# Kernel tuning notes

Hardware: AMD Instinct MI355X
Metric: run time of the kernel (lower is better)

The kernel has to match this reference:

```python
import jax, jax.numpy as jnp
import numpy as np

H = 1024   # hidden_size
B = 4096   # batch
C = 2      # num_classes

def setup_inputs() -> dict:
    key = jax.random.key(0)
    ks = jax.random.split(key, 12)
    s = 0.02
    return {
        "h": jax.random.normal(ks[0], (2, B, H), jnp.float32),
        "c": jax.random.normal(ks[1], (2, B, H), jnp.float32),
        # torch nn.LSTM params: W_ih_l0 (4H, C), W_hh_l0 (4H, H), biases (4H,)
        "W_ih0": jax.random.normal(ks[2], (4 * H, C), jnp.float32) * s,
        "W_hh0": jax.random.normal(ks[3], (4 * H, H), jnp.float32) * s,
        "b_ih0": jax.random.normal(ks[4], (4 * H,), jnp.float32) * s,
        "b_hh0": jax.random.normal(ks[5], (4 * H,), jnp.float32) * s,
        "W_ih1": jax.random.normal(ks[6], (4 * H, H), jnp.float32) * s,
        "W_hh1": jax.random.normal(ks[7], (4 * H, H), jnp.float32) * s,
        "b_ih1": jax.random.normal(ks[8], (4 * H,), jnp.float32) * s,
        "b_hh1": jax.random.normal(ks[9], (4 * H,), jnp.float32) * s,
        "fc_W": jax.random.normal(ks[10], (C, H), jnp.float32) * s,
        "fc_b": jax.random.normal(ks[11], (C,), jnp.float32) * s,
        "pred_len": 64,
    }

def _lstm_cell(gates, c_prev):
    # torch gate order: input, forget, cell(g), output
    i, f, g, o = jnp.split(gates, 4, axis=1)
    c_new = jax.nn.sigmoid(f) * c_prev + jax.nn.sigmoid(i) * jnp.tanh(g)
    h_new = jax.nn.sigmoid(o) * jnp.tanh(c_new)
    return h_new, c_new

def reference(h, c, W_ih0, W_hh0, b_ih0, b_hh0, W_ih1, W_hh1, b_ih1, b_hh1, fc_W, fc_b, pred_len):
    h0, h1 = h[0], h[1]
    c0, c1 = c[0], c[1]
    x0 = jnp.zeros((h0.shape[0], fc_W.shape[0]), h.dtype)  # (B, C)

    def step(carry, _):
        h0, c0, h1, c1, x = carry
        g0 = x @ W_ih0.T + b_ih0 + h0 @ W_hh0.T + b_hh0
        h0n, c0n = _lstm_cell(g0, c0)
        g1 = h0n @ W_ih1.T + b_ih1 + h1 @ W_hh1.T + b_hh1
        h1n, c1n = _lstm_cell(g1, c1)
        logit = h1n @ fc_W.T + fc_b                       # (B, C)
        # greedy argmax feedback (targets=None branch)
        x_next = jax.nn.one_hot(jnp.argmax(logit, axis=1), logit.shape[1], dtype=logit.dtype)
        return (h0n, c0n, h1n, c1n, x_next), logit

    _, logits = jax.lax.scan(step, (h0, c0, h1, c1, x0), None, length=pred_len)
    return jnp.transpose(logits, (1, 0, 2))  # (B, pred_len, C)
```

## Files before the change

### kernel.cpp

```cpp
#include <hip/hip_runtime.h>
#include <stdint.h>

#define H_ 1024
#define NG_ 4096

typedef float f32x4 __attribute__((ext_vector_type(4)));
typedef __bf16 bf16x8 __attribute__((ext_vector_type(8)));

__device__ __forceinline__ unsigned short f2bf(float f) {
  union { float f; uint32_t u; } v; v.f = f;
  uint32_t r = v.u + 0x7FFFu + ((v.u >> 16) & 1u);
  return (unsigned short)(r >> 16);
}
__device__ __forceinline__ float bf2f(unsigned short b) {
  union { uint32_t u; float f; } v; v.u = ((uint32_t)b) << 16; return v.f;
}

__device__ __forceinline__ void gload_lds16(const void* g, void* l) {
  __builtin_amdgcn_global_load_lds(
      (const __attribute__((address_space(1))) void*)g,
      (__attribute__((address_space(3))) void*)l, 16, 0, 0);
}

__device__ __forceinline__ float sigm(float x) { return 1.f / (1.f + __expf(-x)); }
__device__ __forceinline__ float tanh_(float x) { return 1.f - 2.f / (__expf(2.f * x) + 1.f); }

__global__ void prep_w0(const float* __restrict__ Whh0, unsigned short* __restrict__ Wr) {
  int i = (blockIdx.x * 256 + threadIdx.x) * 4;
  int r = i >> 10, k = i & 1023;
  int gate = (r >> 4) & 3;
  int j = ((r >> 6) << 4) + (r & 15);
  const float4 v = *(const float4*)(Whh0 + (size_t)(gate * H_ + j) * H_ + k);
  ushort4 o; o.x = f2bf(v.x); o.y = f2bf(v.y); o.z = f2bf(v.z); o.w = f2bf(v.w);
  *(ushort4*)(Wr + i) = o;
}

__global__ void prep_wcat(const float* __restrict__ Wih1, const float* __restrict__ Whh1,
                          unsigned short* __restrict__ Wr) {
  int i = (blockIdx.x * 256 + threadIdx.x) * 4;
  int r = i >> 11, k = i & 2047;
  int gate = (r >> 4) & 3;
  int j = ((r >> 6) << 4) + (r & 15);
  const float* src = (k < 1024) ? (Wih1 + (size_t)(gate * H_ + j) * H_ + k)
                                : (Whh1 + (size_t)(gate * H_ + j) * H_ + (k - 1024));
  const float4 v = *(const float4*)src;
  ushort4 o; o.x = f2bf(v.x); o.y = f2bf(v.y); o.z = f2bf(v.z); o.w = f2bf(v.w);
  *(ushort4*)(Wr + (size_t)r * 2048 + k) = o;
}

__global__ void prep_small(const float* __restrict__ Wih0,
                           const float* __restrict__ bih0, const float* __restrict__ bhh0,
                           const float* __restrict__ bih1, const float* __restrict__ bhh1,
                           float* __restrict__ bias0r, float* __restrict__ bias1r,
                           float* __restrict__ wi0r) {
  int r = blockIdx.x * 256 + threadIdx.x;
  int gate = (r >> 4) & 3;
  int j = ((r >> 6) << 4) + (r & 15);
  int old = gate * H_ + j;
  bias0r[r] = bih0[old] + bhh0[old];
  bias1r[r] = bih1[old] + bhh1[old];
  wi0r[r * 2 + 0] = Wih0[old * 2 + 0];
  wi0r[r * 2 + 1] = Wih0[old * 2 + 1];
}

__global__ void prep_state(const float* __restrict__ h, const float* __restrict__ c,
                           unsigned short* __restrict__ h0b, unsigned short* __restrict__ h1b,
                           float* __restrict__ c0, float* __restrict__ c1, int bh) {
  int i = (blockIdx.x * 256 + threadIdx.x) * 4;
  float4 a = *(const float4*)(h + i);
  float4 b = *(const float4*)(h + (size_t)bh + i);
  ushort4 oa; oa.x = f2bf(a.x); oa.y = f2bf(a.y); oa.z = f2bf(a.z); oa.w = f2bf(a.w);
  ushort4 ob; ob.x = f2bf(b.x); ob.y = f2bf(b.y); ob.z = f2bf(b.z); ob.w = f2bf(b.w);
  *(ushort4*)(h0b + i) = oa;
  *(ushort4*)(h1b + i) = ob;
  *(float4*)(c0 + i) = *(const float4*)(c + i);
  *(float4*)(c1 + i) = *(const float4*)(c + (size_t)bh + i);
}

__global__ void __launch_bounds__(512, 2)
lstm_gemm_cell(const unsigned short* __restrict__ A0,
               const unsigned short* __restrict__ A1,
               int Ktot,
               const unsigned short* __restrict__ Bw,
               const float* __restrict__ biasr,
               const float* __restrict__ wi0r,
               const int* __restrict__ xidx,
               int have_x,
               float* __restrict__ Cst,
               unsigned short* __restrict__ Hout) {
  __shared__ unsigned short As[2][256 * 64];
  __shared__ unsigned short Bs[2][256 * 64];

  const int tid  = threadIdx.x;
  const int lane = tid & 63;
  const int wv   = tid >> 6;
  const int wm   = wv >> 2;
  const int wn   = wv & 3;
  const int tile_m = blockIdx.y * 256;
  const int tile_n = blockIdx.x * 256;

  const int rowt = tid >> 3;
  const int cb8  = (tid & 7) * 8;
  const int ce   = (((tid & 7) ^ (rowt & 7)) * 8);

  const int NK = Ktot >> 6;

  auto stage = [&](int d, int kt) {
    const int kb = kt << 6;
    const unsigned short* Ap = A0; int kl = kb;
    if (kb >= 1024) { Ap = A1; kl = kb - 1024; }
#pragma unroll
    for (int i = 0; i < 4; ++i) {
      const int row = i * 64 + rowt;
      gload_lds16(Ap + (size_t)(tile_m + row) * H_ + kl + ce, (void*)&As[d][row * 64 + cb8]);
    }
#pragma unroll
    for (int i = 0; i < 4; ++i) {
      const int row = i * 64 + rowt;
      gload_lds16(Bw + (size_t)(tile_n + row) * (size_t)Ktot + kb + ce, (void*)&Bs[d][row * 64 + cb8]);
    }
  };

  f32x4 acc[8][4];
#pragma unroll
  for (int m = 0; m < 8; ++m)
#pragma unroll
    for (int n = 0; n < 4; ++n) acc[m][n] = (f32x4)0.f;

  const int cl  = lane & 15;
  const int khi = lane >> 4;
  const int Xn  = lane & 7;
  const int ksw0 = ((0 + khi) ^ Xn) * 16;
  const int ksw1 = ((4 + khi) ^ Xn) * 16;

  stage(0, 0);
  stage(1, 1);
  asm volatile("s_waitcnt vmcnt(8)" ::: "memory");
  __builtin_amdgcn_sched_barrier(0);
  __builtin_amdgcn_s_barrier();

  for (int kt = 0; kt < NK; ++kt) {
    const int cur = kt & 1;
    const char* Abase = (const char*)&As[cur][0] + (wm * 128 + cl) * 128;
    const char* Bbase = (const char*)&Bs[cur][0] + (wn * 64 + cl) * 128;

    bf16x8 af0[8], af1[8], bf0[4], bf1[4];
#pragma unroll
    for (int m = 0; m < 8; ++m) {
      af0[m] = *(const bf16x8*)(Abase + m * 2048 + ksw0);
      af1[m] = *(const bf16x8*)(Abase + m * 2048 + ksw1);
    }
#pragma unroll
    for (int n = 0; n < 4; ++n) {
      bf0[n] = *(const bf16x8*)(Bbase + n * 2048 + ksw0);
      bf1[n] = *(const bf16x8*)(Bbase + n * 2048 + ksw1);
    }

    asm volatile("s_waitcnt lgkmcnt(0)" ::: "memory");
    __builtin_amdgcn_sched_barrier(0);
    __builtin_amdgcn_s_barrier();

    if (kt + 2 < NK) {
      stage(cur, kt + 2);
      asm volatile("s_waitcnt vmcnt(8)" ::: "memory");
    } else {
      asm volatile("s_waitcnt vmcnt(0)" ::: "memory");
    }
    __builtin_amdgcn_sched_barrier(0);

    __builtin_amdgcn_s_setprio(1);
#pragma unroll
    for (int m = 0; m < 8; ++m)
#pragma unroll
      for (int n = 0; n < 4; ++n)
        acc[m][n] = __builtin_amdgcn_mfma_f32_16x16x32_bf16(af0[m], bf0[n], acc[m][n], 0, 0, 0);
#pragma unroll
    for (int m = 0; m < 8; ++m)
#pragma unroll
      for (int n = 0; n < 4; ++n)
        acc[m][n] = __builtin_amdgcn_mfma_f32_16x16x32_bf16(af1[m], bf1[n], acc[m][n], 0, 0, 0);
    __builtin_amdgcn_s_setprio(0);

    __builtin_amdgcn_s_barrier();
  }

  const int jgrp = (tile_n >> 6) + wn;
  const int j = jgrp * 16 + cl;
  float bias[4], w0v[4] = {0, 0, 0, 0}, w1v[4] = {0, 0, 0, 0};
#pragma unroll
  for (int n = 0; n < 4; ++n) {
    int colr = tile_n + wn * 64 + n * 16 + cl;
    bias[n] = biasr[colr];
    if (have_x) { w0v[n] = wi0r[colr * 2]; w1v[n] = wi0r[colr * 2 + 1]; }
  }
#pragma unroll
  for (int m = 0; m < 8; ++m) {
#pragma unroll
    for (int q = 0; q < 4; ++q) {
      int row = tile_m + wm * 128 + m * 16 + khi * 4 + q;
      float gi = acc[m][0][q] + bias[0];
      float gf = acc[m][1][q] + bias[1];
      float gg = acc[m][2][q] + bias[2];
      float go = acc[m][3][q] + bias[3];
      if (have_x) {
        int x = xidx[row];
        gi += x ? w1v[0] : w0v[0];
        gf += x ? w1v[1] : w0v[1];
        gg += x ? w1v[2] : w0v[2];
        go += x ? w1v[3] : w0v[3];
      }
      size_t off = (size_t)row * H_ + j;
      float cp = Cst[off];
      float cn = sigm(gf) * cp + sigm(gi) * tanh_(gg);
      float hn = sigm(go) * tanh_(cn);
      Cst[off] = cn;
      Hout[off] = f2bf(hn);
    }
  }
}

__global__ void fc_argmax(const unsigned short* __restrict__ h1,
                          const float* __restrict__ fcW, const float* __restrict__ fcb,
                          float* __restrict__ out, int* __restrict__ xidx,
                          int t, int pred_len) {
  const int lane = threadIdx.x & 63;
  const int wv = threadIdx.x >> 6;
  const int row = blockIdx.x * 4 + wv;
  const unsigned short* hp = h1 + (size_t)row * H_ + lane * 16;
  float d0 = 0.f, d1 = 0.f;
#pragma unroll
  for (int u = 0; u < 2; ++u) {
    ushort4 ha = *(const ushort4*)(hp + u * 8);
    ushort4 hb = *(const ushort4*)(hp + u * 8 + 4);
    float hv[8] = { bf2f(ha.x), bf2f(ha.y), bf2f(ha.z), bf2f(ha.w),
                    bf2f(hb.x), bf2f(hb.y), bf2f(hb.z), bf2f(hb.w) };
#pragma unroll
    for (int e = 0; e < 8; ++e) {
      int k = lane * 16 + u * 8 + e;
      d0 += hv[e] * fcW[k];
      d1 += hv[e] * fcW[H_ + k];
    }
  }
#pragma unroll
  for (int off = 32; off > 0; off >>= 1) {
    d0 += __shfl_xor(d0, off);
    d1 += __shfl_xor(d1, off);
  }
  if (lane == 0) {
    d0 += fcb[0]; d1 += fcb[1];
    size_t o = ((size_t)row * pred_len + t) * 2;
    out[o] = d0; out[o + 1] = d1;
    xidx[row] = (d1 > d0) ? 1 : 0;
  }
}

extern "C" void kernel_launch(void* const* d_in, const int* in_sizes, int n_in,
                              void* d_out, int out_size, void* d_ws, size_t ws_size,
                              hipStream_t stream) {
  const float* h     = (const float*)d_in[0];
  const float* c     = (const float*)d_in[1];
  const float* Wih0  = (const float*)d_in[2];
  const float* Whh0  = (const float*)d_in[3];
  const float* bih0  = (const float*)d_in[4];
  const float* bhh0  = (const float*)d_in[5];
  const float* Wih1  = (const float*)d_in[6];
  const float* Whh1  = (const float*)d_in[7];
  const float* bih1  = (const float*)d_in[8];
  const float* bhh1  = (const float*)d_in[9];
  const float* fcW   = (const float*)d_in[10];
  const float* fcb   = (const float*)d_in[11];

  const int B = in_sizes[0] / (2 * H_);
  const int pred_len = out_size / (B * 2);
  const int BH = B * H_;

  size_t off = 0;
  auto carve = [&](size_t bytes) -> void* {
    void* p = (char*)d_ws + off;
    off += (bytes + 255) & ~(size_t)255;
    return p;
  };
  unsigned short* Whh0r = (unsigned short*)carve((size_t)NG_ * 1024 * 2);
  unsigned short* Wcatr = (unsigned short*)carve((size_t)NG_ * 2048 * 2);
  unsigned short* h0b[2], *h1b[2];
  h0b[0] = (unsigned short*)carve((size_t)BH * 2);
  h0b[1] = (unsigned short*)carve((size_t)BH * 2);
  h1b[0] = (unsigned short*)carve((size_t)BH * 2);
  h1b[1] = (unsigned short*)carve((size_t)BH * 2);
  float* c0 = (float*)carve((size_t)BH * 4);
  float* c1 = (float*)carve((size_t)BH * 4);
  float* bias0r = (float*)carve(NG_ * 4);
  float* bias1r = (float*)carve(NG_ * 4);
  float* wi0r   = (float*)carve(NG_ * 2 * 4);
  int*   xidx   = (int*)carve(B * 4);

  hipLaunchKernelGGL(prep_w0,   dim3((NG_ * 1024 / 4) / 256), dim3(256), 0, stream, Whh0, Whh0r);
  hipLaunchKernelGGL(prep_wcat, dim3((NG_ * 2048 / 4) / 256), dim3(256), 0, stream, Wih1, Whh1, Wcatr);
  hipLaunchKernelGGL(prep_small, dim3(NG_ / 256), dim3(256), 0, stream,
                     Wih0, bih0, bhh0, bih1, bhh1, bias0r, bias1r, wi0r);
  hipLaunchKernelGGL(prep_state, dim3((BH / 4) / 256), dim3(256), 0, stream,
                     h, c, h0b[0], h1b[0], c0, c1, BH);

  dim3 ggrid(NG_ / 256, B / 256);
  dim3 gblk(512);
  float* out = (float*)d_out;

  for (int t = 0; t < pred_len; ++t) {
    const int cur = t & 1, nxt = cur ^ 1;
    hipLaunchKernelGGL(lstm_gemm_cell, ggrid, gblk, 0, stream,
                       h0b[cur], (const unsigned short*)nullptr, 1024, Whh0r,
                       bias0r, wi0r, xidx, (t > 0) ? 1 : 0, c0, h0b[nxt]);
    hipLaunchKernelGGL(lstm_gemm_cell, ggrid, gblk, 0, stream,
                       h0b[nxt], h1b[cur], 2048, Wcatr,
                       bias1r, (const float*)nullptr, (const int*)nullptr, 0, c1, h1b[nxt]);
    hipLaunchKernelGGL(fc_argmax, dim3(B / 4), dim3(256), 0, stream,
                       h1b[nxt], fcW, fcb, out, xidx, t, pred_len);
  }
}
```

Baseline: 8.121 ms.

## Restructure GEMM main loop into 8-phase interleaved load/MFMA schedule

Replaces the two-stage per-k-tile loop with an 8-phase schedule per pair of k-tiles. Each phase reads a quarter of the A fragments from LDS, issues half of one A or B global-to-LDS stage, and runs 16 MFMAs, so global loads, LDS reads and compute are interleaved more finely. This aims to hide memory latency and cut register pressure from holding all A fragments at once. In exchange it adds more barriers per k-tile and relies on tight vmcnt accounting. At the tail it re-stages an already consumed tile, which looks questionable.

```diff
diff --git a/kernel.cpp b/kernel.cpp
--- a/kernel.cpp
+++ b/kernel.cpp
@@ -105,18 +105,23 @@
 
   const int NK = Ktot >> 6;
 
-  auto stage = [&](int d, int kt) {
-    const int kb = kt << 6;
+  auto stageA = [&](int t, int half) {
+    const int d = t & 1;
+    const int kb = t << 6;
     const unsigned short* Ap = A0; int kl = kb;
     if (kb >= 1024) { Ap = A1; kl = kb - 1024; }
 #pragma unroll
-    for (int i = 0; i < 4; ++i) {
-      const int row = i * 64 + rowt;
+    for (int i = 0; i < 2; ++i) {
+      const int row = half * 128 + i * 64 + rowt;
       gload_lds16(Ap + (size_t)(tile_m + row) * H_ + kl + ce, (void*)&As[d][row * 64 + cb8]);
     }
-#pragma unroll
-    for (int i = 0; i < 4; ++i) {
-      const int row = i * 64 + rowt;
+  };
+  auto stageB = [&](int t, int half) {
+    const int d = t & 1;
+    const int kb = t << 6;
+#pragma unroll
+    for (int i = 0; i < 2; ++i) {
+      const int row = half * 128 + i * 64 + rowt;
       gload_lds16(Bw + (size_t)(tile_n + row) * (size_t)Ktot + kb + ce, (void*)&Bs[d][row * 64 + cb8]);
     }
   };
@@ -133,56 +138,67 @@
   const int ksw0 = ((0 + khi) ^ Xn) * 16;
   const int ksw1 = ((4 + khi) ^ Xn) * 16;
 
-  stage(0, 0);
-  stage(1, 1);
-  asm volatile("s_waitcnt vmcnt(8)" ::: "memory");
+  bf16x8 bfr0[4], bfr1[4];
+
+#define DO_PHASE(T_, Q_, LOADB_, STAGE_EXPR_, TAILWAIT_)                          \
+  {                                                                               \
+    const char* Ab_ = (const char*)&As[(T_) & 1][0] + (wm * 128 + cl) * 128;      \
+    bf16x8 a00_ = *(const bf16x8*)(Ab_ + (2 * (Q_) + 0) * 2048 + ksw0);           \
+    bf16x8 a01_ = *(const bf16x8*)(Ab_ + (2 * (Q_) + 0) * 2048 + ksw1);           \
+    bf16x8 a10_ = *(const bf16x8*)(Ab_ + (2 * (Q_) + 1) * 2048 + ksw0);           \
+    bf16x8 a11_ = *(const bf16x8*)(Ab_ + (2 * (Q_) + 1) * 2048 + ksw1);           \
+    if (LOADB_) {                                                                 \
+      const char* Bb_ = (const char*)&Bs[(T_) & 1][0] + (wn * 64 + cl) * 128;     \
+      _Pragma("unroll")                                                           \
+      for (int n_ = 0; n_ < 4; ++n_) {                                            \
+        bfr0[n_] = *(const bf16x8*)(Bb_ + n_ * 2048 + ksw0);                      \
+        bfr1[n_] = *(const bf16x8*)(Bb_ + n_ * 2048 + ksw1);                      \
+      }                                                                           \
+    }                                                                             \
+    STAGE_EXPR_;                                                                  \
+    __builtin_amdgcn_s_barrier();                                                 \
+    asm volatile("s_waitcnt lgkmcnt(0)" ::: "memory");                            \
+    __builtin_amdgcn_sched_barrier(0);                                            \
+    __builtin_amdgcn_s_setprio(1);                                                \
+    _Pragma("unroll")                                                             \
+    for (int n_ = 0; n_ < 4; ++n_) {                                              \
+      acc[2*(Q_)+0][n_] = __builtin_amdgcn_mfma_f32_16x16x32_bf16(a00_, bfr0[n_], acc[2*(Q_)+0][n_], 0, 0, 0); \
+      acc[2*(Q_)+0][n_] = __builtin_amdgcn_mfma_f32_16x16x32_bf16(a01_, bfr1[n_], acc[2*(Q_)+0][n_], 0, 0, 0); \
+      acc[2*(Q_)+1][n_] = __builtin_amdgcn_mfma_f32_16x16x32_bf16(a10_, bfr0[n_], acc[2*(Q_)+1][n_], 0, 0, 0); \
+      acc[2*(Q_)+1][n_] = __builtin_amdgcn_mfma_f32_16x16x32_bf16(a11_, bfr1[n_], acc[2*(Q_)+1][n_], 0, 0, 0); \
+    }                                                                             \
+    __builtin_amdgcn_s_setprio(0);                                                \
+    if (TAILWAIT_) {                                                              \
+      asm volatile("s_waitcnt vmcnt(4)" ::: "memory");                            \
+      __builtin_amdgcn_sched_barrier(0);                                          \
+    }                                                                             \
+    __builtin_amdgcn_s_barrier();                                                 \
+  }
+
+  stageA(0, 0); stageA(0, 1);
+  stageB(0, 0); stageB(0, 1);
+  stageB(1, 0); stageB(1, 1);
+  asm volatile("s_waitcnt vmcnt(4)" ::: "memory");
   __builtin_amdgcn_sched_barrier(0);
   __builtin_amdgcn_s_barrier();
 
-  for (int kt = 0; kt < NK; ++kt) {
-    const int cur = kt & 1;
-    const char* Abase = (const char*)&As[cur][0] + (wm * 128 + cl) * 128;
-    const char* Bbase = (const char*)&Bs[cur][0] + (wn * 64 + cl) * 128;
-
-    bf16x8 af0[8], af1[8], bf0[4], bf1[4];
-#pragma unroll
-    for (int m = 0; m < 8; ++m) {
-      af0[m] = *(const bf16x8*)(Abase + m * 2048 + ksw0);
-      af1[m] = *(const bf16x8*)(Abase + m * 2048 + ksw1);
-    }
-#pragma unroll
-    for (int n = 0; n < 4; ++n) {
-      bf0[n] = *(const bf16x8*)(Bbase + n * 2048 + ksw0);
-      bf1[n] = *(const bf16x8*)(Bbase + n * 2048 + ksw1);
-    }
-
-    asm volatile("s_waitcnt lgkmcnt(0)" ::: "memory");
-    __builtin_amdgcn_sched_barrier(0);
-    __builtin_amdgcn_s_barrier();
-
-    if (kt + 2 < NK) {
-      stage(cur, kt + 2);
-      asm volatile("s_waitcnt vmcnt(8)" ::: "memory");
-    } else {
-      asm volatile("s_waitcnt vmcnt(0)" ::: "memory");
-    }
-    __builtin_amdgcn_sched_barrier(0);
-
-    __builtin_amdgcn_s_setprio(1);
-#pragma unroll
-    for (int m = 0; m < 8; ++m)
-#pragma unroll
-      for (int n = 0; n < 4; ++n)
-        acc[m][n] = __builtin_amdgcn_mfma_f32_16x16x32_bf16(af0[m], bf0[n], acc[m][n], 0, 0, 0);
-#pragma unroll
-    for (int m = 0; m < 8; ++m)
-#pragma unroll
-      for (int n = 0; n < 4; ++n)
-        acc[m][n] = __builtin_amdgcn_mfma_f32_16x16x32_bf16(af1[m], bf1[n], acc[m][n], 0, 0, 0);
-    __builtin_amdgcn_s_setprio(0);
-
-    __builtin_amdgcn_s_barrier();
-  }
+  const int NIT = NK >> 1;
+  for (int j = 0; j < NIT; ++j) {
+    const int t0 = 2 * j, t1 = 2 * j + 1;
+    const int t2 = (t0 + 2 < NK) ? t0 + 2 : t0;
+    const int t3 = (t1 + 2 < NK) ? t1 + 2 : t1;
+    DO_PHASE(t0, 0, 1, stageA(t1, 0), 0);
+    DO_PHASE(t0, 1, 0, stageA(t1, 1), 0);
+    DO_PHASE(t0, 2, 0, stageB(t2, 0), 0);
+    DO_PHASE(t0, 3, 0, stageB(t2, 1), 1);
+    DO_PHASE(t1, 0, 1, stageA(t2, 0), 0);
+    DO_PHASE(t1, 1, 0, stageA(t2, 1), 0);
+    DO_PHASE(t1, 2, 0, stageB(t3, 0), 0);
+    DO_PHASE(t1, 3, 0, stageB(t3, 1), 1);
+  }
+#undef DO_PHASE
+
+  asm volatile("s_waitcnt vmcnt(0)" ::: "memory");
 
   const int jgrp = (tile_n >> 6) + wn;
   const int j = jgrp * 16 + cl;
```

Result: no change. 8.042 ms (-1.0%).

## Interleave LDS fragment loads with MFMA in a four-phase ping-pong GEMM pipeline

Applied to the files above, without the earlier changes.

Restructures the GEMM main loop into four sub-phases, each issuing half-tile A global→LDS loads or B loads and prefetching the next register fragments while MFMAs run on the current ones. Register fragment arrays are halved, with A/B ping-pong buffers across phases. The aim is to hide LDS read latency and the global load issue behind matrix-core work instead of stalling on lgkmcnt(0) before every K step. It adds more barriers and uses clamped dummy stage indices in the tail iterations, which makes the buffer hazard reasoning fragile.

```diff
diff --git a/kernel.cpp b/kernel.cpp
--- a/kernel.cpp
+++ b/kernel.cpp
@@ -105,18 +105,23 @@
 
   const int NK = Ktot >> 6;
 
-  auto stage = [&](int d, int kt) {
-    const int kb = kt << 6;
+  auto stageA = [&](int v, int half) {
+    const int d = v & 1;
+    const int kb = v << 6;
     const unsigned short* Ap = A0; int kl = kb;
     if (kb >= 1024) { Ap = A1; kl = kb - 1024; }
 #pragma unroll
-    for (int i = 0; i < 4; ++i) {
-      const int row = i * 64 + rowt;
+    for (int i = 0; i < 2; ++i) {
+      const int row = half * 128 + i * 64 + rowt;
       gload_lds16(Ap + (size_t)(tile_m + row) * H_ + kl + ce, (void*)&As[d][row * 64 + cb8]);
     }
-#pragma unroll
-    for (int i = 0; i < 4; ++i) {
-      const int row = i * 64 + rowt;
+  };
+  auto stageB = [&](int v, int half) {
+    const int d = v & 1;
+    const int kb = v << 6;
+#pragma unroll
+    for (int i = 0; i < 2; ++i) {
+      const int row = half * 128 + i * 64 + rowt;
       gload_lds16(Bw + (size_t)(tile_n + row) * (size_t)Ktot + kb + ce, (void*)&Bs[d][row * 64 + cb8]);
     }
   };
@@ -129,60 +134,86 @@
 
   const int cl  = lane & 15;
   const int khi = lane >> 4;
-  const int Xn  = lane & 7;
-  const int ksw0 = ((0 + khi) ^ Xn) * 16;
-  const int ksw1 = ((4 + khi) ^ Xn) * 16;
-
-  stage(0, 0);
-  stage(1, 1);
-  asm volatile("s_waitcnt vmcnt(8)" ::: "memory");
+  const int ksw0 = ((0 + khi) ^ (cl & 7)) * 16;
+  const int ksw1 = ((4 + khi) ^ (cl & 7)) * 16;
+
+  const char* Ab0 = (const char*)&As[0][0] + (wm * 128 + cl) * 128;
+  const char* Bb0 = (const char*)&Bs[0][0] + (wn * 64 + cl) * 128;
+
+  bf16x8 aX[4], aY[4], bX[4], bY[4];
+
+#define MFMA16(AF, BF, MOFF)                                                         \
+  _Pragma("unroll")                                                                  \
+  for (int n_ = 0; n_ < 4; ++n_)                                                     \
+  _Pragma("unroll")                                                                  \
+  for (int i_ = 0; i_ < 4; ++i_)                                                     \
+    acc[(MOFF) + i_][n_] =                                                           \
+        __builtin_amdgcn_mfma_f32_16x16x32_bf16(AF[i_], BF[n_], acc[(MOFF) + i_][n_], 0, 0, 0);
+
+  stageA(0, 0); stageA(0, 1);
+  stageB(0, 0); stageB(0, 1);
+  stageB(1, 0); stageB(1, 1);
+  asm volatile("s_waitcnt vmcnt(4)" ::: "memory");
   __builtin_amdgcn_sched_barrier(0);
   __builtin_amdgcn_s_barrier();
-
-  for (int kt = 0; kt < NK; ++kt) {
-    const int cur = kt & 1;
-    const char* Abase = (const char*)&As[cur][0] + (wm * 128 + cl) * 128;
-    const char* Bbase = (const char*)&Bs[cur][0] + (wn * 64 + cl) * 128;
-
-    bf16x8 af0[8], af1[8], bf0[4], bf1[4];
-#pragma unroll
-    for (int m = 0; m < 8; ++m) {
-      af0[m] = *(const bf16x8*)(Abase + m * 2048 + ksw0);
-      af1[m] = *(const bf16x8*)(Abase + m * 2048 + ksw1);
-    }
-#pragma unroll
-    for (int n = 0; n < 4; ++n) {
-      bf0[n] = *(const bf16x8*)(Bbase + n * 2048 + ksw0);
-      bf1[n] = *(const bf16x8*)(Bbase + n * 2048 + ksw1);
-    }
-
-    asm volatile("s_waitcnt lgkmcnt(0)" ::: "memory");
+#pragma unroll
+  for (int i = 0; i < 4; ++i) aX[i] = *(const bf16x8*)(Ab0 + i * 2048 + ksw0);
+#pragma unroll
+  for (int n = 0; n < 4; ++n) bX[n] = *(const bf16x8*)(Bb0 + n * 2048 + ksw0);
+
+  for (int u = 0; u < NK; ++u) {
+    const char* Ab = Ab0 + (u & 1) * 32768;
+    const char* Bb = Bb0 + (u & 1) * 32768;
+    const int un = (u + 1 < NK) ? u + 1 : NK - 2;
+    const int ub = (u + 2 < NK) ? u + 2 : (((u + 2) & 1) ? NK - 1 : NK - 2);
+    const int ur = (u + 1 < NK) ? u + 1 : u;
+    const char* Abn = Ab0 + (ur & 1) * 32768;
+    const char* Bbn = Bb0 + (ur & 1) * 32768;
+
+#pragma unroll
+    for (int i = 0; i < 4; ++i) aY[i] = *(const bf16x8*)(Ab + 8192 + i * 2048 + ksw0);
+    stageA(un, 0);
+    __builtin_amdgcn_s_barrier();
+    __builtin_amdgcn_s_setprio(1);
+    MFMA16(aX, bX, 0);
+    __builtin_amdgcn_s_setprio(0);
+    __builtin_amdgcn_s_barrier();
+
+#pragma unroll
+    for (int i = 0; i < 4; ++i) aX[i] = *(const bf16x8*)(Ab + i * 2048 + ksw1);
+#pragma unroll
+    for (int n = 0; n < 4; ++n) bY[n] = *(const bf16x8*)(Bb + n * 2048 + ksw1);
+    stageA(un, 1);
+    __builtin_amdgcn_s_barrier();
+    __builtin_amdgcn_s_setprio(1);
+    MFMA16(aY, bX, 4);
+    __builtin_amdgcn_s_setprio(0);
+    __builtin_amdgcn_s_barrier();
+
+#pragma unroll
+    for (int i = 0; i < 4; ++i) aY[i] = *(const bf16x8*)(Ab + 8192 + i * 2048 + ksw1);
+    __builtin_amdgcn_s_barrier();
+    __builtin_amdgcn_s_setprio(1);
+    MFMA16(aX, bY, 0);
+    __builtin_amdgcn_s_setprio(0);
+    __builtin_amdgcn_s_barrier();
+
+    stageB(ub, 0); stageB(ub, 1);
+    asm volatile("s_waitcnt vmcnt(4)" ::: "memory");
     __builtin_amdgcn_sched_barrier(0);
     __builtin_amdgcn_s_barrier();
-
-    if (kt + 2 < NK) {
-      stage(cur, kt + 2);
-      asm volatile("s_waitcnt vmcnt(8)" ::: "memory");
-    } else {
-      asm volatile("s_waitcnt vmcnt(0)" ::: "memory");
-    }
-    __builtin_amdgcn_sched_barrier(0);
-
+#pragma unroll
+    for (int i = 0; i < 4; ++i) aX[i] = *(const bf16x8*)(Abn + i * 2048 + ksw0);
+#pragma unroll
+    for (int n = 0; n < 4; ++n) bX[n] = *(const bf16x8*)(Bbn + n * 2048 + ksw0);
     __builtin_amdgcn_s_setprio(1);
-#pragma unroll
-    for (int m = 0; m < 8; ++m)
-#pragma unroll
-      for (int n = 0; n < 4; ++n)
-        acc[m][n] = __builtin_amdgcn_mfma_f32_16x16x32_bf16(af0[m], bf0[n], acc[m][n], 0, 0, 0);
-#pragma unroll
-    for (int m = 0; m < 8; ++m)
-#pragma unroll
-      for (int n = 0; n < 4; ++n)
-        acc[m][n] = __builtin_amdgcn_mfma_f32_16x16x32_bf16(af1[m], bf1[n], acc[m][n], 0, 0, 0);
+    MFMA16(aY, bY, 4);
     __builtin_amdgcn_s_setprio(0);
-
-    __builtin_amdgcn_s_barrier();
-  }
+    __builtin_amdgcn_s_barrier();
+  }
+#undef MFMA16
+
+  asm volatile("s_waitcnt vmcnt(0) lgkmcnt(0)" ::: "memory");
 
   const int jgrp = (tile_n >> 6) + wn;
   const int j = jgrp * 16 + cl;
```

Result: slower. 9.221 ms (+13.5%).

## Load weight fragments directly from global memory and halve the N tile

Applied to the files above, without the earlier changes.

The GEMM-cell kernel no longer stages weight tiles in LDS. Each wave reads its bf16 weight fragments straight from global memory, while only the activation tile goes through double-buffered LDS. The N tile shrinks from 256 to 128, giving twice as many blocks, and launch bounds are raised to allow 4 blocks per CU with a smaller accumulator set. Nontemporal stores are used for the bf16 weights, state and h outputs. The trade-off is fewer LDS bytes and more occupancy against uncoalesced 16-byte global reads of weights and less reuse per block.

```diff
diff --git a/kernel.cpp b/kernel.cpp
--- a/kernel.cpp
+++ b/kernel.cpp
@@ -6,6 +6,7 @@
 
 typedef float f32x4 __attribute__((ext_vector_type(4)));
 typedef __bf16 bf16x8 __attribute__((ext_vector_type(8)));
+typedef unsigned short us4 __attribute__((ext_vector_type(4)));
 
 __device__ __forceinline__ unsigned short f2bf(float f) {
   union { float f; uint32_t u; } v; v.f = f;
@@ -31,8 +32,8 @@
   int gate = (r >> 4) & 3;
   int j = ((r >> 6) << 4) + (r & 15);
   const float4 v = *(const float4*)(Whh0 + (size_t)(gate * H_ + j) * H_ + k);
-  ushort4 o; o.x = f2bf(v.x); o.y = f2bf(v.y); o.z = f2bf(v.z); o.w = f2bf(v.w);
-  *(ushort4*)(Wr + i) = o;
+  us4 o; o.x = f2bf(v.x); o.y = f2bf(v.y); o.z = f2bf(v.z); o.w = f2bf(v.w);
+  __builtin_nontemporal_store(o, (us4*)(Wr + i));
 }
 
 __global__ void prep_wcat(const float* __restrict__ Wih1, const float* __restrict__ Whh1,
@@ -44,8 +45,8 @@
   const float* src = (k < 1024) ? (Wih1 + (size_t)(gate * H_ + j) * H_ + k)
                                 : (Whh1 + (size_t)(gate * H_ + j) * H_ + (k - 1024));
   const float4 v = *(const float4*)src;
-  ushort4 o; o.x = f2bf(v.x); o.y = f2bf(v.y); o.z = f2bf(v.z); o.w = f2bf(v.w);
-  *(ushort4*)(Wr + (size_t)r * 2048 + k) = o;
+  us4 o; o.x = f2bf(v.x); o.y = f2bf(v.y); o.z = f2bf(v.z); o.w = f2bf(v.w);
+  __builtin_nontemporal_store(o, (us4*)(Wr + (size_t)r * 2048 + k));
 }
 
 __global__ void prep_small(const float* __restrict__ Wih0,
@@ -69,15 +70,15 @@
   int i = (blockIdx.x * 256 + threadIdx.x) * 4;
   float4 a = *(const float4*)(h + i);
   float4 b = *(const float4*)(h + (size_t)bh + i);
-  ushort4 oa; oa.x = f2bf(a.x); oa.y = f2bf(a.y); oa.z = f2bf(a.z); oa.w = f2bf(a.w);
-  ushort4 ob; ob.x = f2bf(b.x); ob.y = f2bf(b.y); ob.z = f2bf(b.z); ob.w = f2bf(b.w);
-  *(ushort4*)(h0b + i) = oa;
-  *(ushort4*)(h1b + i) = ob;
+  us4 oa; oa.x = f2bf(a.x); oa.y = f2bf(a.y); oa.z = f2bf(a.z); oa.w = f2bf(a.w);
+  us4 ob; ob.x = f2bf(b.x); ob.y = f2bf(b.y); ob.z = f2bf(b.z); ob.w = f2bf(b.w);
+  __builtin_nontemporal_store(oa, (us4*)(h0b + i));
+  __builtin_nontemporal_store(ob, (us4*)(h1b + i));
   *(float4*)(c0 + i) = *(const float4*)(c + i);
   *(float4*)(c1 + i) = *(const float4*)(c + (size_t)bh + i);
 }
 
-__global__ void __launch_bounds__(512, 2)
+__global__ void __launch_bounds__(512, 4)
 lstm_gemm_cell(const unsigned short* __restrict__ A0,
                const unsigned short* __restrict__ A1,
                int Ktot,
@@ -89,15 +90,14 @@
                float* __restrict__ Cst,
                unsigned short* __restrict__ Hout) {
   __shared__ unsigned short As[2][256 * 64];
-  __shared__ unsigned short Bs[2][256 * 64];
 
   const int tid  = threadIdx.x;
   const int lane = tid & 63;
   const int wv   = tid >> 6;
-  const int wm   = wv >> 2;
-  const int wn   = wv & 3;
+  const int wm   = wv >> 1;
+  const int wn   = wv & 1;
   const int tile_m = blockIdx.y * 256;
-  const int tile_n = blockIdx.x * 256;
+  const int tile_n = blockIdx.x * 128;
 
   const int rowt = tid >> 3;
   const int cb8  = (tid & 7) * 8;
@@ -105,8 +105,9 @@
 
   const int NK = Ktot >> 6;
 
-  auto stage = [&](int d, int kt) {
-    const int kb = kt << 6;
+  auto stageA = [&](int v) {
+    const int d = v & 1;
+    const int kb = v << 6;
     const unsigned short* Ap = A0; int kl = kb;
     if (kb >= 1024) { Ap = A1; kl = kb - 1024; }
 #pragma unroll
@@ -114,73 +115,65 @@
       const int row = i * 64 + rowt;
       gload_lds16(Ap + (size_t)(tile_m + row) * H_ + kl + ce, (void*)&As[d][row * 64 + cb8]);
     }
-#pragma unroll
-    for (int i = 0; i < 4; ++i) {
-      const int row = i * 64 + rowt;
-      gload_lds16(Bw + (size_t)(tile_n + row) * (size_t)Ktot + kb + ce, (void*)&Bs[d][row * 64 + cb8]);
-    }
   };
 
-  f32x4 acc[8][4];
-#pragma unroll
-  for (int m = 0; m < 8; ++m)
+  f32x4 acc[4][4];
+#pragma unroll
+  for (int m = 0; m < 4; ++m)
 #pragma unroll
     for (int n = 0; n < 4; ++n) acc[m][n] = (f32x4)0.f;
 
   const int cl  = lane & 15;
   const int khi = lane >> 4;
-  const int Xn  = lane & 7;
-  const int ksw0 = ((0 + khi) ^ Xn) * 16;
-  const int ksw1 = ((4 + khi) ^ Xn) * 16;
-
-  stage(0, 0);
-  stage(1, 1);
-  asm volatile("s_waitcnt vmcnt(8)" ::: "memory");
+  const int ksw0 = ((0 + khi) ^ (cl & 7)) * 16;
+  const int ksw1 = ((4 + khi) ^ (cl & 7)) * 16;
+
+  const size_t Kb2 = (size_t)Ktot * 2;
+  const char* Bbase = (const char*)Bw + (size_t)(tile_n + wn * 64 + cl) * Kb2 + khi * 16;
+  const size_t Bn = 16 * Kb2;
+
+  stageA(0);
+  asm volatile("s_waitcnt vmcnt(0)" ::: "memory");
   __builtin_amdgcn_sched_barrier(0);
   __builtin_amdgcn_s_barrier();
 
-  for (int kt = 0; kt < NK; ++kt) {
-    const int cur = kt & 1;
-    const char* Abase = (const char*)&As[cur][0] + (wm * 128 + cl) * 128;
-    const char* Bbase = (const char*)&Bs[cur][0] + (wn * 64 + cl) * 128;
-
-    bf16x8 af0[8], af1[8], bf0[4], bf1[4];
-#pragma unroll
-    for (int m = 0; m < 8; ++m) {
-      af0[m] = *(const bf16x8*)(Abase + m * 2048 + ksw0);
-      af1[m] = *(const bf16x8*)(Abase + m * 2048 + ksw1);
-    }
-#pragma unroll
-    for (int n = 0; n < 4; ++n) {
-      bf0[n] = *(const bf16x8*)(Bbase + n * 2048 + ksw0);
-      bf1[n] = *(const bf16x8*)(Bbase + n * 2048 + ksw1);
-    }
-
-    asm volatile("s_waitcnt lgkmcnt(0)" ::: "memory");
+  for (int u = 0; u < NK; ++u) {
+    const char* Ab = (const char*)&As[u & 1][0] + (wm * 64 + cl) * 128;
+    const char* Bu = Bbase + (size_t)u * 128;
+
+    bf16x8 bX[4];
+#pragma unroll
+    for (int n = 0; n < 4; ++n) bX[n] = *(const bf16x8*)(Bu + (size_t)n * Bn);
+    if (u + 1 < NK) stageA(u + 1);
     __builtin_amdgcn_sched_barrier(0);
-    __builtin_amdgcn_s_barrier();
-
-    if (kt + 2 < NK) {
-      stage(cur, kt + 2);
-      asm volatile("s_waitcnt vmcnt(8)" ::: "memory");
-    } else {
-      asm volatile("s_waitcnt vmcnt(0)" ::: "memory");
-    }
+
+    bf16x8 aX[4];
+#pragma unroll
+    for (int m = 0; m < 4; ++m) aX[m] = *(const bf16x8*)(Ab + m * 2048 + ksw0);
+    __builtin_amdgcn_s_setprio(1);
+#pragma unroll
+    for (int m = 0; m < 4; ++m)
+#pragma unroll
+      for (int n = 0; n < 4; ++n)
+        acc[m][n] = __builtin_amdgcn_mfma_f32_16x16x32_bf16(aX[m], bX[n], acc[m][n], 0, 0, 0);
+    __builtin_amdgcn_s_setprio(0);
+
+    bf16x8 bY[4];
+#pragma unroll
+    for (int n = 0; n < 4; ++n) bY[n] = *(const bf16x8*)(Bu + (size_t)n * Bn + 64);
+    bf16x8 aY[4];
+#pragma unroll
+    for (int m = 0; m < 4; ++m) aY[m] = *(const bf16x8*)(Ab + m * 2048 + ksw1);
+    __builtin_amdgcn_s_setprio(1);
+#pragma unroll
+    for (int m = 0; m < 4; ++m)
+#pragma unroll
+      for (int n = 0; n < 4; ++n)
+        acc[m][n] = __builtin_amdgcn_mfma_f32_16x16x32_bf16(aY[m], bY[n], acc[m][n], 0, 0, 0);
+    __builtin_amdgcn_s_setprio(0);
+
+    asm volatile("s_waitcnt vmcnt(0)" ::: "memory");
     __builtin_amdgcn_sched_barrier(0);
-
-    __builtin_amdgcn_s_setprio(1);
-#pragma unroll
-    for (int m = 0; m < 8; ++m)
-#pragma unroll
-      for (int n = 0; n < 4; ++n)
-        acc[m][n] = __builtin_amdgcn_mfma_f32_16x16x32_bf16(af0[m], bf0[n], acc[m][n], 0, 0, 0);
-#pragma unroll
-    for (int m = 0; m < 8; ++m)
-#pragma unroll
-      for (int n = 0; n < 4; ++n)
-        acc[m][n] = __builtin_amdgcn_mfma_f32_16x16x32_bf16(af1[m], bf1[n], acc[m][n], 0, 0, 0);
-    __builtin_amdgcn_s_setprio(0);
-
     __builtin_amdgcn_s_barrier();
   }
 
@@ -194,10 +187,10 @@
     if (have_x) { w0v[n] = wi0r[colr * 2]; w1v[n] = wi0r[colr * 2 + 1]; }
   }
 #pragma unroll
-  for (int m = 0; m < 8; ++m) {
+  for (int m = 0; m < 4; ++m) {
 #pragma unroll
     for (int q = 0; q < 4; ++q) {
-      int row = tile_m + wm * 128 + m * 16 + khi * 4 + q;
+      int row = tile_m + wm * 64 + m * 16 + khi * 4 + q;
       float gi = acc[m][0][q] + bias[0];
       float gf = acc[m][1][q] + bias[1];
       float gg = acc[m][2][q] + bias[2];
@@ -214,7 +207,7 @@
       float cn = sigm(gf) * cp + sigm(gi) * tanh_(gg);
       float hn = sigm(go) * tanh_(cn);
       Cst[off] = cn;
-      Hout[off] = f2bf(hn);
+      __builtin_nontemporal_store(f2bf(hn), Hout + off);
     }
   }
 }
@@ -301,7 +294,7 @@
   hipLaunchKernelGGL(prep_state, dim3((BH / 4) / 256), dim3(256), 0, stream,
                      h, c, h0b[0], h1b[0], c0, c1, BH);
 
-  dim3 ggrid(NG_ / 256, B / 256);
+  dim3 ggrid(NG_ / 128, B / 256);
   dim3 gblk(512);
   float* out = (float*)d_out;
 
```

Result: slower. 16.95 ms (+108.7%).
